# Kernel tuning notes

Measured on AMD Instinct MI355X. Metric: run time of the kernel, lower is better.

Reference implementation:

```python
import jax, jax.numpy as jnp
import numpy as np

EMBED_DIM = 512
NUM_HEADS = 8
HEAD_DIM = EMBED_DIM // NUM_HEADS
SCALE = HEAD_DIM ** -0.5
TEMP = 1.0


def setup_inputs() -> dict:
    key = jax.random.key(0)
    ks = jax.random.split(key, 12)
    B, N, Nk, C = 4, 2048, 2048, EMBED_DIM
    s = C ** -0.5
    return {
        "x": jax.random.normal(ks[0], (B, N, C), jnp.float32),
        "y": jax.random.normal(ks[1], (B, Nk, C), jnp.float32),
        "z": jax.random.normal(ks[2], (B, Nk, C), jnp.float32),
        "Wq": jax.random.normal(ks[3], (C, C), jnp.float32) * s,
        "bq": jnp.zeros((C,), jnp.float32),
        "Wk": jax.random.normal(ks[4], (C, C), jnp.float32) * s,
        "bk": jnp.zeros((C,), jnp.float32),
        "Wv": jax.random.normal(ks[5], (C, C), jnp.float32) * s,
        "bv": jnp.zeros((C,), jnp.float32),
        "Wo": jax.random.normal(ks[6], (C, C), jnp.float32) * s,
        "bo": jnp.zeros((C,), jnp.float32),
    }


def reference(x, y, z, Wq, bq, Wk, bk, Wv, bv, Wo, bo):
    B, N, C = x.shape
    Nk = y.shape[1]
    H, D = NUM_HEADS, HEAD_DIM

    def split_heads(t, L):
        return t.reshape(B, L, H, D).transpose(0, 2, 1, 3)  # [B,H,L,D]

    q = split_heads(x @ Wq.T + bq, N)
    k = split_heads(y @ Wk.T + bk, Nk)
    v = split_heads(z @ Wv.T + bv, Nk)

    # [B,H,N,Nk] logits, scaled
    logits = jnp.einsum("bhnd,bhkd->bhnk", q, k) * SCALE

    # Gumbel-softmax (soft, tau=TEMP) with a fixed noise key
    gkey = jax.random.key(42)
    gumbels = jax.random.gumbel(gkey, logits.shape, logits.dtype)
    attn = jax.nn.softmax((logits + gumbels) / TEMP, axis=-1)

    out = jnp.einsum("bhnk,bhkd->bhnd", attn, v)
    out = out.transpose(0, 2, 1, 3).reshape(B, N, C)
    return out @ Wo.T + bo
```

## Files before the change

kernel.cpp:

```cpp
#include <hip/hip_runtime.h>
#include <hip/hip_bf16.h>
#include <stdint.h>

#define Bdim 4
#define Hdim 8
#define Ndim 2048
#define Cdim 512
#define Ddim 64
#define SCALE_F 0.125f
#define KSPLIT 4
#define LOG2E 1.44269504f

typedef __bf16 bf16_t;
typedef __bf16 bf16x8 __attribute__((ext_vector_type(8)));
typedef float f32x4 __attribute__((ext_vector_type(4)));

#define SWZ_XOR_F(v, m) \
  __int_as_float(__builtin_amdgcn_ds_swizzle(__float_as_int(v), (0x1F | ((m) << 10))))

__device__ __forceinline__ float gumbel_pfac(uint32_t flat) {
  const uint32_t k0 = 0u, k1 = 42u, k2 = 0x1BD11BDAu ^ 0u ^ 42u;
  uint32_t x0 = 0u;
  uint32_t x1 = flat;
  x0 += k0; x1 += k1;
#define TF_R(r) { x0 += x1; x1 = __builtin_rotateleft32(x1, r); x1 ^= x0; }
#define TF_R4A TF_R(13) TF_R(15) TF_R(26) TF_R(6)
#define TF_R4B TF_R(17) TF_R(29) TF_R(16) TF_R(24)
  TF_R4A  x0 += k1; x1 += k2 + 1u;
  TF_R4B  x0 += k2; x1 += k0 + 2u;
  TF_R4A  x0 += k0; x1 += k1 + 3u;
  TF_R4B  x0 += k1; x1 += k2 + 4u;
  TF_R4A  x0 += k2; x1 += k0 + 5u;
#undef TF_R4B
#undef TF_R4A
#undef TF_R
  uint32_t bits = x0 ^ x1;
  float f = __uint_as_float((bits >> 9) | 0x3F800000u) - 1.0f;
  float u = f + 1.17549435e-38f;
  return -__builtin_amdgcn_rcpf(__builtin_amdgcn_logf(u));
}

__global__ void cvt_f32_bf16(const float* __restrict__ in,
                             bf16_t* __restrict__ out, int n8) {
  int i = blockIdx.x * blockDim.x + threadIdx.x;
  if (i < n8) {
    const float4* p = (const float4*)in + (size_t)i * 2;
    float4 a = p[0], b = p[1];
    union { bf16_t h[8]; uint4 u; } pk;
    pk.h[0] = (bf16_t)a.x; pk.h[1] = (bf16_t)a.y;
    pk.h[2] = (bf16_t)a.z; pk.h[3] = (bf16_t)a.w;
    pk.h[4] = (bf16_t)b.x; pk.h[5] = (bf16_t)b.y;
    pk.h[6] = (bf16_t)b.z; pk.h[7] = (bf16_t)b.w;
    *((uint4*)out + i) = pk.u;
  }
}

__device__ __forceinline__ void gemm_core(const bf16_t* __restrict__ A,
                                          const bf16_t* __restrict__ W,
                                          int m0, int n0,
                                          bf16_t* As, bf16_t* Ws,
                                          f32x4 (&acc)[4][4]) {
  const int t = threadIdx.x;
  const int wave = t >> 6, lane = t & 63;
  const int ln = lane & 15, qd = lane >> 4;
  const int wm = wave >> 1, wn = wave & 1;

#pragma unroll
  for (int i = 0; i < 4; i++)
#pragma unroll
    for (int j = 0; j < 4; j++) acc[i][j] = (f32x4){0.f, 0.f, 0.f, 0.f};

  for (int kt = 0; kt < Cdim / 64; ++kt) {
#pragma unroll
    for (int it = 0; it < 4; ++it) {
      int vec = it * 256 + t;
      int row = vec >> 3, c8 = (vec & 7) * 8;
      *(bf16x8*)&As[row * 72 + c8] =
          *(const bf16x8*)&A[(size_t)(m0 + row) * Cdim + kt * 64 + c8];
      *(bf16x8*)&Ws[row * 72 + c8] =
          *(const bf16x8*)&W[(size_t)(n0 + row) * Cdim + kt * 64 + c8];
    }
    __syncthreads();
#pragma unroll
    for (int ks = 0; ks < 2; ++ks) {
      bf16x8 af[4], bfr[4];
#pragma unroll
      for (int i = 0; i < 4; i++)
        af[i] = *(const bf16x8*)&As[(wm * 64 + i * 16 + ln) * 72 + ks * 32 + qd * 8];
#pragma unroll
      for (int j = 0; j < 4; j++)
        bfr[j] = *(const bf16x8*)&Ws[(wn * 64 + j * 16 + ln) * 72 + ks * 32 + qd * 8];
#pragma unroll
      for (int i = 0; i < 4; i++)
#pragma unroll
        for (int j = 0; j < 4; j++)
          acc[i][j] = __builtin_amdgcn_mfma_f32_16x16x32_bf16(af[i], bfr[j],
                                                              acc[i][j], 0, 0, 0);
    }
    __syncthreads();
  }
}

__global__ __launch_bounds__(256, 2)
void qkv_gemm_kernel(const bf16_t* __restrict__ xb, const bf16_t* __restrict__ yb,
                     const bf16_t* __restrict__ zb, const bf16_t* __restrict__ wqb,
                     const bf16_t* __restrict__ wkb, const bf16_t* __restrict__ wvb,
                     const float* __restrict__ bq, const float* __restrict__ bk,
                     const float* __restrict__ bv, bf16_t* __restrict__ qo,
                     bf16_t* __restrict__ ko, bf16_t* __restrict__ vo) {
  __shared__ bf16_t As[128 * 72];
  __shared__ bf16_t Ws[128 * 72];
  const int sel = blockIdx.z;
  const bf16_t* A = sel == 0 ? xb : (sel == 1 ? yb : zb);
  const bf16_t* W = sel == 0 ? wqb : (sel == 1 ? wkb : wvb);
  const float* bias = sel == 0 ? bq : (sel == 1 ? bk : bv);
  bf16_t* O = sel == 0 ? qo : (sel == 1 ? ko : vo);
  const float mul = sel == 0 ? SCALE_F : 1.0f;
  const int m0 = blockIdx.y * 128, n0 = blockIdx.x * 128;

  f32x4 acc[4][4];
  gemm_core(A, W, m0, n0, As, Ws, acc);

  const int t = threadIdx.x;
  const int wave = t >> 6, lane = t & 63;
  const int ln = lane & 15, qd = lane >> 4;
  const int wm = wave >> 1, wn = wave & 1;
#pragma unroll
  for (int i = 0; i < 4; i++)
#pragma unroll
    for (int j = 0; j < 4; j++)
#pragma unroll
      for (int r = 0; r < 4; r++) {
        int grow = m0 + wm * 64 + i * 16 + qd * 4 + r;
        int gcol = n0 + wn * 64 + j * 16 + ln;
        float val = (acc[i][j][r] + bias[gcol]) * mul;
        int b = grow >> 11, n = grow & 2047;
        int h = gcol >> 6, d = gcol & 63;
        O[(((size_t)b * Hdim + h) * Ndim + n) * Ddim + d] = (bf16_t)val;
      }
}

__global__ __launch_bounds__(256, 2)
void out_gemm_kernel(const bf16_t* __restrict__ ab, const bf16_t* __restrict__ wob,
                     const float* __restrict__ bo, float* __restrict__ out) {
  __shared__ bf16_t As[128 * 72];
  __shared__ bf16_t Ws[128 * 72];
  const int m0 = blockIdx.y * 128, n0 = blockIdx.x * 128;
  f32x4 acc[4][4];
  gemm_core(ab, wob, m0, n0, As, Ws, acc);

  const int t = threadIdx.x;
  const int wave = t >> 6, lane = t & 63;
  const int ln = lane & 15, qd = lane >> 4;
  const int wm = wave >> 1, wn = wave & 1;
#pragma unroll
  for (int i = 0; i < 4; i++)
#pragma unroll
    for (int j = 0; j < 4; j++)
#pragma unroll
      for (int r = 0; r < 4; r++) {
        int grow = m0 + wm * 64 + i * 16 + qd * 4 + r;
        int gcol = n0 + wn * 64 + j * 16 + ln;
        out[(size_t)grow * Cdim + gcol] = acc[i][j][r] + bo[gcol];
      }
}

__global__ __launch_bounds__(256, 4)
void attn_kernel(const bf16_t* __restrict__ qb, const bf16_t* __restrict__ kb,
                 const bf16_t* __restrict__ vb, bf16_t* __restrict__ part_o,
                 float* __restrict__ part_l) {
  __shared__ bf16_t Ks[64 * 72];
  __shared__ bf16_t Vt[64 * 72];
  __shared__ bf16_t Ps[64 * 72];

  const int t = threadIdx.x;
  const int wave = t >> 6, lane = t & 63;
  const int ln = lane & 15, qd = lane >> 4;
  const int qtile = blockIdx.x;
  const int bh = blockIdx.y;
  const int z = blockIdx.z;
  const int qbase = qtile * 64;
  const int kt_lo = z * (Ndim / 64 / KSPLIT);
  const int kt_hi = kt_lo + (Ndim / 64 / KSPLIT);

  const bf16_t* Qg = qb + (size_t)bh * Ndim * Ddim;
  const bf16_t* Kg = kb + (size_t)bh * Ndim * Ddim;
  const bf16_t* Vg = vb + (size_t)bh * Ndim * Ddim;

  const bf16_t* Qrow = Qg + (size_t)(qbase + wave * 16 + ln) * Ddim;
  bf16x8 qf0 = *(const bf16x8*)&Qrow[qd * 8];
  bf16x8 qf1 = *(const bf16x8*)&Qrow[32 + qd * 8];

  const int row0 = t >> 3,        c80 = (t & 7) * 8;
  const int row1 = (256 + t) >> 3, c81 = ((256 + t) & 7) * 8;
  const int swz0 = ((row0 >> 3) ^ (c80 >> 3)) * 8 + (row0 & 7);
  const int swz1 = ((row1 >> 3) ^ (c81 >> 3)) * 8 + (row1 & 7);

  bf16x8 kr0 = *(const bf16x8*)&Kg[(size_t)(kt_lo * 64 + row0) * Ddim + c80];
  bf16x8 kr1 = *(const bf16x8*)&Kg[(size_t)(kt_lo * 64 + row1) * Ddim + c81];
  bf16x8 vr0 = *(const bf16x8*)&Vg[(size_t)(kt_lo * 64 + row0) * Ddim + c80];
  bf16x8 vr1 = *(const bf16x8*)&Vg[(size_t)(kt_lo * 64 + row1) * Ddim + c81];

  float l_r[4] = {0.f, 0.f, 0.f, 0.f};
  f32x4 o_acc[4];
#pragma unroll
  for (int j = 0; j < 4; j++) o_acc[j] = (f32x4){0.f, 0.f, 0.f, 0.f};

  const uint32_t flat_bh = (uint32_t)bh << 22;

  for (int kt = kt_lo; kt < kt_hi; ++kt) {
    *(bf16x8*)&Ks[row0 * 72 + c80] = kr0;
    *(bf16x8*)&Ks[row1 * 72 + c81] = kr1;
#pragma unroll
    for (int jj = 0; jj < 8; jj++) Vt[(c80 + jj) * 72 + swz0] = vr0[jj];
#pragma unroll
    for (int jj = 0; jj < 8; jj++) Vt[(c81 + jj) * 72 + swz1] = vr1[jj];
    __syncthreads();

    if (kt + 1 < kt_hi) {
      kr0 = *(const bf16x8*)&Kg[(size_t)((kt + 1) * 64 + row0) * Ddim + c80];
      kr1 = *(const bf16x8*)&Kg[(size_t)((kt + 1) * 64 + row1) * Ddim + c81];
      vr0 = *(const bf16x8*)&Vg[(size_t)((kt + 1) * 64 + row0) * Ddim + c80];
      vr1 = *(const bf16x8*)&Vg[(size_t)((kt + 1) * 64 + row1) * Ddim + c81];
    }

    f32x4 s[4];
#pragma unroll
    for (int j = 0; j < 4; j++) s[j] = (f32x4){0.f, 0.f, 0.f, 0.f};
#pragma unroll
    for (int j = 0; j < 4; j++) {
      bf16x8 bk0 = *(const bf16x8*)&Ks[(j * 16 + ln) * 72 + qd * 8];
      bf16x8 bk1 = *(const bf16x8*)&Ks[(j * 16 + ln) * 72 + 32 + qd * 8];
      s[j] = __builtin_amdgcn_mfma_f32_16x16x32_bf16(qf0, bk0, s[j], 0, 0, 0);
      s[j] = __builtin_amdgcn_mfma_f32_16x16x32_bf16(qf1, bk1, s[j], 0, 0, 0);
    }

#pragma unroll
    for (int r = 0; r < 4; r++) {
      int qrow = qbase + wave * 16 + qd * 4 + r;
      uint32_t fbase = flat_bh + ((uint32_t)qrow << 11) + (uint32_t)(kt * 64 + ln);
#pragma unroll
      for (int j = 0; j < 4; j++) {
        float pf = gumbel_pfac(fbase + j * 16);
        float pv = __builtin_amdgcn_exp2f(s[j][r] * LOG2E) * pf;
        l_r[r] += pv;
        Ps[(wave * 16 + qd * 4 + r) * 72 + j * 16 + ln] = (bf16_t)pv;
      }
    }

#pragma unroll
    for (int ks = 0; ks < 2; ++ks) {
      bf16x8 af = *(const bf16x8*)&Ps[(wave * 16 + ln) * 72 + ks * 32 + qd * 8];
#pragma unroll
      for (int j = 0; j < 4; j++) {
        int d = j * 16 + ln;
        bf16x8 bv8 = *(const bf16x8*)&Vt[d * 72 + (((ks * 4 + qd) ^ (d >> 3)) << 3)];
        o_acc[j] = __builtin_amdgcn_mfma_f32_16x16x32_bf16(af, bv8, o_acc[j], 0, 0, 0);
      }
    }
    __syncthreads();
  }

  const int pidx = ((bh << 5) | qtile) * KSPLIT + z;
  bf16_t* po = part_o + (size_t)pidx * 64 * 64;
  float* pl = part_l + (size_t)pidx * 64;

#pragma unroll
  for (int r = 0; r < 4; r++) {
    float lsum = l_r[r];
    lsum += SWZ_XOR_F(lsum, 1);
    lsum += SWZ_XOR_F(lsum, 2);
    lsum += SWZ_XOR_F(lsum, 4);
    lsum += SWZ_XOR_F(lsum, 8);
    if (ln == 0) pl[wave * 16 + qd * 4 + r] = lsum;
  }
#pragma unroll
  for (int j = 0; j < 4; j++)
#pragma unroll
    for (int r = 0; r < 4; r++) {
      int row = wave * 16 + qd * 4 + r;
      int col = j * 16 + ln;
      po[row * 64 + col] = (bf16_t)o_acc[j][r];
    }
}

__global__ __launch_bounds__(256, 8)
void attn_combine(const bf16_t* __restrict__ part_o,
                  const float* __restrict__ part_l, bf16_t* __restrict__ ab) {
  const int blk = blockIdx.x;
  const int bh = blk >> 5, qtile = blk & 31;
  const int t = threadIdx.x;
  const int row = t >> 2, c0 = (t & 3) * 16;

  float l = 0.f;
#pragma unroll
  for (int zz = 0; zz < KSPLIT; zz++)
    l += part_l[(size_t)(blk * KSPLIT + zz) * 64 + row];
  const float linv = 1.0f / l;

  float acc[16];
#pragma unroll
  for (int i = 0; i < 16; i++) acc[i] = 0.f;
#pragma unroll
  for (int zz = 0; zz < KSPLIT; zz++) {
    const bf16_t* po =
        part_o + (size_t)(blk * KSPLIT + zz) * 64 * 64 + row * 64 + c0;
    bf16x8 a0 = *(const bf16x8*)&po[0];
    bf16x8 a1 = *(const bf16x8*)&po[8];
#pragma unroll
    for (int i = 0; i < 8; i++) { acc[i] += (float)a0[i]; acc[8 + i] += (float)a1[i]; }
  }

  const int b = bh >> 3, h = bh & 7;
  bf16_t* dst = ab + ((size_t)b * Ndim + qtile * 64 + row) * Cdim + h * 64 + c0;
  union { bf16_t h8[8]; uint4 u; } pk0, pk1;
#pragma unroll
  for (int i = 0; i < 8; i++) {
    pk0.h8[i] = (bf16_t)(acc[i] * linv);
    pk1.h8[i] = (bf16_t)(acc[8 + i] * linv);
  }
  *(uint4*)&dst[0] = pk0.u;
  *(uint4*)&dst[8] = pk1.u;
}

extern "C" void kernel_launch(void* const* d_in, const int* in_sizes, int n_in,
                              void* d_out, int out_size, void* d_ws, size_t ws_size,
                              hipStream_t stream) {
  const float* x  = (const float*)d_in[0];
  const float* y  = (const float*)d_in[1];
  const float* z  = (const float*)d_in[2];
  const float* Wq = (const float*)d_in[3];
  const float* bq = (const float*)d_in[4];
  const float* Wk = (const float*)d_in[5];
  const float* bk = (const float*)d_in[6];
  const float* Wv = (const float*)d_in[7];
  const float* bv = (const float*)d_in[8];
  const float* Wo = (const float*)d_in[9];
  const float* bo = (const float*)d_in[10];
  float* out = (float*)d_out;

  bf16_t* base = (bf16_t*)d_ws;
  const size_t NBIG = (size_t)Bdim * Ndim * Cdim;
  const size_t NW   = (size_t)Cdim * Cdim;
  bf16_t* xb  = base;
  bf16_t* yb  = xb + NBIG;
  bf16_t* zb  = yb + NBIG;
  bf16_t* wqb = zb + NBIG;
  bf16_t* wkb = wqb + NW;
  bf16_t* wvb = wkb + NW;
  bf16_t* wob = wvb + NW;
  bf16_t* qb  = wob + NW;
  bf16_t* kb  = qb + NBIG;
  bf16_t* vb  = kb + NBIG;
  bf16_t* ab  = vb + NBIG;
  bf16_t* part_o = ab + NBIG;
  float* part_l = (float*)(part_o + (size_t)1024 * KSPLIT * 64 * 64);

  int n8b = (int)(NBIG / 8), n8w = (int)(NW / 8);
  cvt_f32_bf16<<<n8b / 256, 256, 0, stream>>>(x, xb, n8b);
  cvt_f32_bf16<<<n8b / 256, 256, 0, stream>>>(y, yb, n8b);
  cvt_f32_bf16<<<n8b / 256, 256, 0, stream>>>(z, zb, n8b);
  cvt_f32_bf16<<<n8w / 256, 256, 0, stream>>>(Wq, wqb, n8w);
  cvt_f32_bf16<<<n8w / 256, 256, 0, stream>>>(Wk, wkb, n8w);
  cvt_f32_bf16<<<n8w / 256, 256, 0, stream>>>(Wv, wvb, n8w);
  cvt_f32_bf16<<<n8w / 256, 256, 0, stream>>>(Wo, wob, n8w);

  qkv_gemm_kernel<<<dim3(Cdim / 128, (Bdim * Ndim) / 128, 3), 256, 0, stream>>>(
      xb, yb, zb, wqb, wkb, wvb, bq, bk, bv, qb, kb, vb);

  attn_kernel<<<dim3(Ndim / 64, Bdim * Hdim, KSPLIT), 256, 0, stream>>>(
      qb, kb, vb, part_o, part_l);

  attn_combine<<<dim3(1024), 256, 0, stream>>>(part_o, part_l, ab);

  out_gemm_kernel<<<dim3(Cdim / 128, (Bdim * Ndim) / 128), 256, 0, stream>>>(
      ab, wob, bo, out);
}
```

Baseline: 439.0 us.

## Fold log2e into Q scale, reuse K smem for P, compute rowsum via MFMA

Folds the log2e factor into the Q projection scale so the attention loop drops a multiply per score. P now reuses the K shared-memory tile, which needs an extra barrier per iteration but lowers LDS use and may raise occupancy. The row-sum of P is computed by an MFMA against a ones vector instead of per-element float adds and a swizzle reduction, so the sum now comes from the bf16-rounded P. The Gumbel uniform is built with a single v_alignbit instruction and the tiny epsilon add is dropped, which could give log(0) when the mantissa bits are all zero.

Result: no change. 432.8 us (-1.4%).

```diff
diff --git a/kernel.cpp b/kernel.cpp
--- a/kernel.cpp
+++ b/kernel.cpp
@@ -10,13 +10,11 @@
 #define SCALE_F 0.125f
 #define KSPLIT 4
 #define LOG2E 1.44269504f
+#define QSCALE_F (SCALE_F * LOG2E)
 
 typedef __bf16 bf16_t;
 typedef __bf16 bf16x8 __attribute__((ext_vector_type(8)));
 typedef float f32x4 __attribute__((ext_vector_type(4)));
-
-#define SWZ_XOR_F(v, m) \
-  __int_as_float(__builtin_amdgcn_ds_swizzle(__float_as_int(v), (0x1F | ((m) << 10))))
 
 __device__ __forceinline__ float gumbel_pfac(uint32_t flat) {
   const uint32_t k0 = 0u, k1 = 42u, k2 = 0x1BD11BDAu ^ 0u ^ 42u;
@@ -35,8 +33,9 @@
 #undef TF_R4A
 #undef TF_R
   uint32_t bits = x0 ^ x1;
-  float f = __uint_as_float((bits >> 9) | 0x3F800000u) - 1.0f;
-  float u = f + 1.17549435e-38f;
+  uint32_t mant;
+  asm("v_alignbit_b32 %0, %1, %2, 9" : "=v"(mant) : "s"(127u), "v"(bits));
+  float u = __uint_as_float(mant) - 1.0f;
   return -__builtin_amdgcn_rcpf(__builtin_amdgcn_logf(u));
 }
 
@@ -115,7 +114,7 @@
   const bf16_t* W = sel == 0 ? wqb : (sel == 1 ? wkb : wvb);
   const float* bias = sel == 0 ? bq : (sel == 1 ? bk : bv);
   bf16_t* O = sel == 0 ? qo : (sel == 1 ? ko : vo);
-  const float mul = sel == 0 ? SCALE_F : 1.0f;
+  const float mul = sel == 0 ? QSCALE_F : 1.0f;
   const int m0 = blockIdx.y * 128, n0 = blockIdx.x * 128;
 
   f32x4 acc[4][4];
@@ -169,9 +168,8 @@
 void attn_kernel(const bf16_t* __restrict__ qb, const bf16_t* __restrict__ kb,
                  const bf16_t* __restrict__ vb, bf16_t* __restrict__ part_o,
                  float* __restrict__ part_l) {
-  __shared__ bf16_t Ks[64 * 72];
+  __shared__ bf16_t KPs[64 * 72];
   __shared__ bf16_t Vt[64 * 72];
-  __shared__ bf16_t Ps[64 * 72];
 
   const int t = threadIdx.x;
   const int wave = t >> 6, lane = t & 63;
@@ -191,6 +189,11 @@
   bf16x8 qf0 = *(const bf16x8*)&Qrow[qd * 8];
   bf16x8 qf1 = *(const bf16x8*)&Qrow[32 + qd * 8];
 
+  const bf16_t one_h = (bf16_t)1.0f;
+  bf16x8 ones;
+#pragma unroll
+  for (int i = 0; i < 8; i++) ones[i] = one_h;
+
   const int row0 = t >> 3,        c80 = (t & 7) * 8;
   const int row1 = (256 + t) >> 3, c81 = ((256 + t) & 7) * 8;
   const int swz0 = ((row0 >> 3) ^ (c80 >> 3)) * 8 + (row0 & 7);
@@ -201,7 +204,7 @@
   bf16x8 vr0 = *(const bf16x8*)&Vg[(size_t)(kt_lo * 64 + row0) * Ddim + c80];
   bf16x8 vr1 = *(const bf16x8*)&Vg[(size_t)(kt_lo * 64 + row1) * Ddim + c81];
 
-  float l_r[4] = {0.f, 0.f, 0.f, 0.f};
+  f32x4 l_acc = (f32x4){0.f, 0.f, 0.f, 0.f};
   f32x4 o_acc[4];
 #pragma unroll
   for (int j = 0; j < 4; j++) o_acc[j] = (f32x4){0.f, 0.f, 0.f, 0.f};
@@ -209,8 +212,8 @@
   const uint32_t flat_bh = (uint32_t)bh << 22;
 
   for (int kt = kt_lo; kt < kt_hi; ++kt) {
-    *(bf16x8*)&Ks[row0 * 72 + c80] = kr0;
-    *(bf16x8*)&Ks[row1 * 72 + c81] = kr1;
+    *(bf16x8*)&KPs[row0 * 72 + c80] = kr0;
+    *(bf16x8*)&KPs[row1 * 72 + c81] = kr1;
 #pragma unroll
     for (int jj = 0; jj < 8; jj++) Vt[(c80 + jj) * 72 + swz0] = vr0[jj];
 #pragma unroll
@@ -229,11 +232,12 @@
     for (int j = 0; j < 4; j++) s[j] = (f32x4){0.f, 0.f, 0.f, 0.f};
 #pragma unroll
     for (int j = 0; j < 4; j++) {
-      bf16x8 bk0 = *(const bf16x8*)&Ks[(j * 16 + ln) * 72 + qd * 8];
-      bf16x8 bk1 = *(const bf16x8*)&Ks[(j * 16 + ln) * 72 + 32 + qd * 8];
+      bf16x8 bk0 = *(const bf16x8*)&KPs[(j * 16 + ln) * 72 + qd * 8];
+      bf16x8 bk1 = *(const bf16x8*)&KPs[(j * 16 + ln) * 72 + 32 + qd * 8];
       s[j] = __builtin_amdgcn_mfma_f32_16x16x32_bf16(qf0, bk0, s[j], 0, 0, 0);
       s[j] = __builtin_amdgcn_mfma_f32_16x16x32_bf16(qf1, bk1, s[j], 0, 0, 0);
     }
+    __syncthreads();
 
 #pragma unroll
     for (int r = 0; r < 4; r++) {
@@ -242,15 +246,15 @@
 #pragma unroll
       for (int j = 0; j < 4; j++) {
         float pf = gumbel_pfac(fbase + j * 16);
-        float pv = __builtin_amdgcn_exp2f(s[j][r] * LOG2E) * pf;
-        l_r[r] += pv;
-        Ps[(wave * 16 + qd * 4 + r) * 72 + j * 16 + ln] = (bf16_t)pv;
+        float pv = __builtin_amdgcn_exp2f(s[j][r]) * pf;
+        KPs[(wave * 16 + qd * 4 + r) * 72 + j * 16 + ln] = (bf16_t)pv;
       }
     }
 
 #pragma unroll
     for (int ks = 0; ks < 2; ++ks) {
-      bf16x8 af = *(const bf16x8*)&Ps[(wave * 16 + ln) * 72 + ks * 32 + qd * 8];
+      bf16x8 af = *(const bf16x8*)&KPs[(wave * 16 + ln) * 72 + ks * 32 + qd * 8];
+      l_acc = __builtin_amdgcn_mfma_f32_16x16x32_bf16(af, ones, l_acc, 0, 0, 0);
 #pragma unroll
       for (int j = 0; j < 4; j++) {
         int d = j * 16 + ln;
@@ -265,14 +269,9 @@
   bf16_t* po = part_o + (size_t)pidx * 64 * 64;
   float* pl = part_l + (size_t)pidx * 64;
 
-#pragma unroll
-  for (int r = 0; r < 4; r++) {
-    float lsum = l_r[r];
-    lsum += SWZ_XOR_F(lsum, 1);
-    lsum += SWZ_XOR_F(lsum, 2);
-    lsum += SWZ_XOR_F(lsum, 4);
-    lsum += SWZ_XOR_F(lsum, 8);
-    if (ln == 0) pl[wave * 16 + qd * 4 + r] = lsum;
+  if (ln == 0) {
+#pragma unroll
+    for (int r = 0; r < 4; r++) pl[wave * 16 + qd * 4 + r] = l_acc[r];
   }
 #pragma unroll
   for (int j = 0; j < 4; j++)
```
